# Kernel optimization log

Measured on AMD Instinct MI355X. Metric: run time of the kernel, lower is better.

The kernel has to match this reference:

```python
import jax, jax.numpy as jnp
import numpy as np

DIM = 1024
NUM_HEADS = 16
HEAD_DIM = DIM // NUM_HEADS
SCALE = HEAD_DIM ** -0.5
NEG = -1e9


def setup_inputs() -> dict:
    key = jax.random.key(0)
    ks = jax.random.split(key, 10)
    B, N, M, C = 8, 1024, 1024, DIM
    q = jax.random.normal(ks[0], (B, N, C), jnp.float32)
    k = jax.random.normal(ks[1], (B, M, C), jnp.float32)
    v = jax.random.normal(ks[2], (B, M, C), jnp.float32)
    mask = jax.random.randint(ks[3], (B, N), 0, 2, jnp.int32)
    target_mask = jax.random.randint(ks[4], (B, N, M), 0, 2, jnp.int32)
    Wq = jax.random.normal(ks[5], (C, C), jnp.float32) * 0.02
    Wk = jax.random.normal(ks[6], (C, C), jnp.float32) * 0.02
    Wv = jax.random.normal(ks[7], (C, C), jnp.float32) * 0.02
    Wo = jax.random.normal(ks[8], (C, C), jnp.float32) * 0.02
    bo = jnp.zeros((C,), jnp.float32)
    return {"q": q, "k": k, "v": v, "mask": mask, "target_mask": target_mask,
            "Wq": Wq, "Wk": Wk, "Wv": Wv, "Wo": Wo, "bo": bo}


def reference(q, k, v, mask, target_mask, Wq, Wk, Wv, Wo, bo):
    B, N, C = q.shape
    M = k.shape[1]
    H, D = NUM_HEADS, HEAD_DIM
    qh = (q @ Wq).reshape(B, N, H, D)
    kh = (k @ Wk).reshape(B, M, H, D)
    vh = (v @ Wv).reshape(B, M, H, D)
    attn = jnp.einsum('bnhd,bmhd->bhnm', qh, kh) * SCALE  # (B,H,N,M)
    # self-attn key mask (B,N) -> broadcast over queries (requires N==M as in original)
    attn = jnp.where(mask[:, None, None, :] == 0, NEG, attn)
    # cross-attn mask (B,N,M) -> broadcast over heads
    attn = jnp.where(target_mask[:, None, :, :] == 0, NEG, attn)
    attn = jax.nn.softmax(attn, axis=-1)
    x = jnp.einsum('bhnm,bmhd->bnhd', attn, vh).reshape(B, N, C)
    return x @ Wo + bo
```

## Files before the change

### kernel.cpp

```cpp
#include <hip/hip_runtime.h>
#include <hip/hip_bf16.h>

#define DEV __device__ __forceinline__

typedef __attribute__((ext_vector_type(8))) short bf16x8;
typedef __attribute__((ext_vector_type(4))) float f32x4;
typedef unsigned int u32;
typedef unsigned long long u64;

DEV short f2bf(float f) {
  union { float f; u32 u; } x; x.f = f;
  u32 r = x.u + 0x7fffu + ((x.u >> 16) & 1u);
  return (short)(r >> 16);
}

DEV void gload_lds16(const void* g, void* l) {
  __builtin_amdgcn_global_load_lds(
      (const __attribute__((address_space(1))) u32*)g,
      (__attribute__((address_space(3))) u32*)l, 16, 0, 0);
}

DEV void stage_t128(const char* base, int ktb, char* lds, int w, int lane) {
  int r8 = lane >> 3;
  int csw = ((lane & 7) ^ r8) << 4;
#pragma unroll
  for (int i = 0; i < 4; ++i) {
    int c = w * 4 + i;
    gload_lds16(base + (size_t)(c * 8 + r8) * 2048 + ktb + csw, lds + c * 1024);
  }
}

DEV bf16x8 frag(const short* L, int row, int col) {
  return *(const bf16x8*)&L[row * 64 + (col ^ ((row & 7) << 3))];
}

__global__ __launch_bounds__(256) void aconv(const float* __restrict__ q,
    const float* __restrict__ k, const float* __restrict__ v,
    short* __restrict__ qb, short* __restrict__ kb, short* __restrict__ vb) {
  const float* src; short* dst;
  if (blockIdx.z == 0)      { src = q; dst = qb; }
  else if (blockIdx.z == 1) { src = k; dst = kb; }
  else                      { src = v; dst = vb; }
  size_t i = ((size_t)blockIdx.x * 256 + threadIdx.x) * 8;
  float4 f0 = *(const float4*)(src + i);
  float4 f1 = *(const float4*)(src + i + 4);
  bf16x8 o;
  o[0] = f2bf(f0.x); o[1] = f2bf(f0.y); o[2] = f2bf(f0.z); o[3] = f2bf(f0.w);
  o[4] = f2bf(f1.x); o[5] = f2bf(f1.y); o[6] = f2bf(f1.z); o[7] = f2bf(f1.w);
  *(bf16x8*)(dst + i) = o;
}

__global__ __launch_bounds__(256) void pack_mask(const int* __restrict__ mask,
                                                 const int* __restrict__ tmask,
                                                 u64* __restrict__ pk) {
  int bn = blockIdx.x;
  int b = bn >> 10;
  int t = threadIdx.x, w = t >> 6, lane = t & 63;
  const int* tr = tmask + (size_t)bn * 1024;
  const int* mr = mask + b * 1024;
#pragma unroll
  for (int it = 0; it < 4; ++it) {
    int m = it * 256 + w * 64 + lane;
    bool on = (mr[m] != 0) && (tr[m] != 0);
    u64 bits = __ballot(on);
    if (lane == 0) pk[(size_t)bn * 16 + it * 4 + w] = bits;
  }
}

__global__ __launch_bounds__(256) void wconv4(const float* __restrict__ W0,
    const float* __restrict__ W1, const float* __restrict__ W2,
    const float* __restrict__ W3, short* __restrict__ WtAll) {
  const float* W = blockIdx.z == 0 ? W0 : blockIdx.z == 1 ? W1
                 : blockIdx.z == 2 ? W2 : W3;
  short* Wt = WtAll + (size_t)blockIdx.z * 1024 * 1024;
  __shared__ short tile[64][65];
  int k0 = blockIdx.x * 64, n0 = blockIdx.y * 64;
  int t = threadIdx.x;
  int r = t >> 2, c = (t & 3) * 16;
  const float* src = W + (size_t)(k0 + r) * 1024 + n0 + c;
#pragma unroll
  for (int i = 0; i < 16; i += 4) {
    float4 f = *(const float4*)(src + i);
    tile[r][c + i + 0] = f2bf(f.x);
    tile[r][c + i + 1] = f2bf(f.y);
    tile[r][c + i + 2] = f2bf(f.z);
    tile[r][c + i + 3] = f2bf(f.w);
  }
  __syncthreads();
  bf16x8 v0, v1;
#pragma unroll
  for (int i = 0; i < 8; ++i) v0[i] = tile[c + i][r];
#pragma unroll
  for (int i = 0; i < 8; ++i) v1[i] = tile[c + 8 + i][r];
  short* dst = Wt + (size_t)(n0 + r) * 1024 + k0 + c;
  *(bf16x8*)(dst) = v0;
  *(bf16x8*)(dst + 8) = v1;
}

__global__ __launch_bounds__(256) void vtrans(const short* __restrict__ vh,
                                              short* __restrict__ vht) {
  __shared__ short tile[64][65];
  int m0 = blockIdx.x * 64;
  int bh = blockIdx.y;
  int t = threadIdx.x;
  int r = t >> 2, c = (t & 3) * 16;
  const short* src = vh + ((size_t)bh * 1024 + m0 + r) * 64 + c;
  bf16x8 a0 = *(const bf16x8*)(src);
  bf16x8 a1 = *(const bf16x8*)(src + 8);
#pragma unroll
  for (int i = 0; i < 8; ++i) tile[r][c + i] = a0[i];
#pragma unroll
  for (int i = 0; i < 8; ++i) tile[r][c + 8 + i] = a1[i];
  __syncthreads();
  bf16x8 v0, v1;
#pragma unroll
  for (int i = 0; i < 8; ++i) v0[i] = tile[c + i][r];
#pragma unroll
  for (int i = 0; i < 8; ++i) v1[i] = tile[c + 8 + i][r];
  short* dst = vht + ((size_t)bh * 64 + r) * 1024 + m0 + c;
  *(bf16x8*)dst = v0;
  *(bf16x8*)(dst + 8) = v1;
}

#define QSCALE 0.18033688011112042f

__global__ __launch_bounds__(256, 2) void gemm_qkv(
    const short* __restrict__ qb, const short* __restrict__ kb, const short* __restrict__ vb,
    const short* __restrict__ WtAll,
    short* __restrict__ qh, short* __restrict__ kh, short* __restrict__ vh) {
  int flat = blockIdx.z * 512 + blockIdx.y * 8 + blockIdx.x;
  int nid = (flat & 7) * 192 + (flat >> 3);
  int zz = nid >> 9;
  int rr = nid & 511;
  int bm = (rr >> 3) * 128, bn = (rr & 7) * 128;

  const short* A; short* Ch; float cs;
  if (zz == 0)      { A = qb; Ch = qh; cs = QSCALE; }
  else if (zz == 1) { A = kb; Ch = kh; cs = 1.0f; }
  else              { A = vb; Ch = vh; cs = 1.0f; }
  const short* Wt = WtAll + (size_t)zz * 1024 * 1024;

  __shared__ __align__(16) short As[128 * 64];
  __shared__ __align__(16) short Bs[128 * 64];

  int tid = threadIdx.x;
  int lane = tid & 63, w = tid >> 6;
  int wm = w >> 1, wn = w & 1;
  int lr = lane & 15, lg = lane >> 4;

  const f32x4 fz = {0.f, 0.f, 0.f, 0.f};
  f32x4 acc[4][4];
#pragma unroll
  for (int i = 0; i < 4; ++i)
#pragma unroll
    for (int j = 0; j < 4; ++j) acc[i][j] = fz;

  const char* abase = (const char*)A + (size_t)bm * 2048;
  const char* bbase = (const char*)Wt + (size_t)bn * 2048;

  for (int ktb = 0; ktb < 2048; ktb += 128) {
    stage_t128(abase, ktb, (char*)As, w, lane);
    stage_t128(bbase, ktb, (char*)Bs, w, lane);
    __syncthreads();
#pragma unroll
    for (int ks = 0; ks < 2; ++ks) {
      bf16x8 af[4], bfr[4];
#pragma unroll
      for (int mi = 0; mi < 4; ++mi)
        af[mi] = frag(As, wm * 64 + mi * 16 + lr, ks * 32 + lg * 8);
#pragma unroll
      for (int ni = 0; ni < 4; ++ni)
        bfr[ni] = frag(Bs, wn * 64 + ni * 16 + lr, ks * 32 + lg * 8);
#pragma unroll
      for (int mi = 0; mi < 4; ++mi)
#pragma unroll
        for (int ni = 0; ni < 4; ++ni)
          acc[mi][ni] = __builtin_amdgcn_mfma_f32_16x16x32_bf16(af[mi], bfr[ni], acc[mi][ni], 0, 0, 0);
    }
    __syncthreads();
  }
#pragma unroll
  for (int mi = 0; mi < 4; ++mi)
#pragma unroll
    for (int ni = 0; ni < 4; ++ni) {
      int ccol = bn + wn * 64 + ni * 16 + lr;
      int h = ccol >> 6, d = ccol & 63;
#pragma unroll
      for (int j = 0; j < 4; ++j) {
        int r = bm + wm * 64 + mi * 16 + lg * 4 + j;
        int bb = r >> 10, n = r & 1023;
        Ch[(((size_t)bb * 16 + h) * 1024 + n) * 64 + d] = f2bf(acc[mi][ni][j] * cs);
      }
    }
}

DEV void stage_kv(const char* kbase, const char* vbase, int kv0,
                  short* Ksb, short* Vsb, int w, int lane) {
#pragma unroll
  for (int i = 0; i < 2; ++i) {
    int c = w * 2 + i;
    int row = (lane >> 3);
    int colb = ((lane & 7) ^ row) << 4;
    gload_lds16(kbase + (size_t)(kv0 + c * 8 + row) * 128 + colb, (char*)Ksb + c * 1024);
    gload_lds16(vbase + (size_t)(c * 8 + row) * 2048 + kv0 * 2 + colb, (char*)Vsb + c * 1024);
  }
}

__global__ __launch_bounds__(256, 2) void attn(
    const short* __restrict__ qh, const short* __restrict__ kh, const short* __restrict__ vht,
    const u64* __restrict__ pk, short* __restrict__ x) {
  __shared__ __align__(16) short Ks[2][4096];
  __shared__ __align__(16) short Vs[2][4096];
  __shared__ __align__(16) short Ps[8192];

  int flat = blockIdx.y * 8 + blockIdx.x;
  int nid = (flat & 7) * 128 + (flat >> 3);
  int bh = nid >> 3, qt = nid & 7;
  int b = bh >> 4;
  int tid = threadIdx.x, lane = tid & 63, w = tid >> 6;
  int lr = lane & 15, lg = lane >> 4;

  bf16x8 qa[2][2];
  {
    const short* qb2 = qh + ((size_t)bh * 1024 + qt * 128 + w * 32) * 64;
#pragma unroll
    for (int mi = 0; mi < 2; ++mi)
#pragma unroll
      for (int ks = 0; ks < 2; ++ks)
        qa[mi][ks] = *(const bf16x8*)(qb2 + (mi * 16 + lr) * 64 + ks * 32 + lg * 8);
  }

  const f32x4 fz = {0.f, 0.f, 0.f, 0.f};
  f32x4 o[2][4];
  float psum[2][4];
#pragma unroll
  for (int mi = 0; mi < 2; ++mi)
#pragma unroll
    for (int j = 0; j < 4; ++j) psum[mi][j] = 0.f;
#pragma unroll
  for (int mi = 0; mi < 2; ++mi)
#pragma unroll
    for (int nd = 0; nd < 4; ++nd) o[mi][nd] = fz;

  const char* kbase = (const char*)(kh + (size_t)bh * 65536);
  const char* vbase = (const char*)(vht + (size_t)bh * 65536);
  const u64* pkb = pk + ((size_t)b * 1024 + qt * 128) * 16;

  stage_kv(kbase, vbase, 0, Ks[0], Vs[0], w, lane);
  __syncthreads();
  int cur = 0;

  for (int t = 0; t < 16; ++t) {
    if (t < 15) stage_kv(kbase, vbase, (t + 1) * 64, Ks[cur ^ 1], Vs[cur ^ 1], w, lane);

    u64 pw[2][4];
#pragma unroll
    for (int mi = 0; mi < 2; ++mi)
#pragma unroll
      for (int j = 0; j < 4; ++j)
        pw[mi][j] = pkb[(w * 32 + mi * 16 + lg * 4 + j) * 16 + t];

    f32x4 s[2][4];
#pragma unroll
    for (int mi = 0; mi < 2; ++mi)
#pragma unroll
      for (int ni = 0; ni < 4; ++ni) s[mi][ni] = fz;
#pragma unroll
    for (int ks = 0; ks < 2; ++ks) {
      bf16x8 kb2[4];
#pragma unroll
      for (int ni = 0; ni < 4; ++ni)
        kb2[ni] = *(const bf16x8*)&Ks[cur][(ni * 16 + lr) * 64 + ((ks * 32 + lg * 8) ^ ((lr & 7) << 3))];
#pragma unroll
      for (int mi = 0; mi < 2; ++mi)
#pragma unroll
        for (int ni = 0; ni < 4; ++ni)
          s[mi][ni] = __builtin_amdgcn_mfma_f32_16x16x32_bf16(qa[mi][ks], kb2[ni], s[mi][ni], 0, 0, 0);
    }

#pragma unroll
    for (int mi = 0; mi < 2; ++mi)
#pragma unroll
      for (int j = 0; j < 4; ++j) {
        u32 lo = (u32)pw[mi][j], hi = (u32)(pw[mi][j] >> 32);
        float rs = 0.f;
#pragma unroll
        for (int ni = 0; ni < 4; ++ni) {
          u32 bit = ((ni < 2 ? lo : hi) >> ((ni & 1) * 16 + lr)) & 1u;
          float e = __builtin_amdgcn_exp2f(s[mi][ni][j]);
          float p = bit ? e : 0.f;
          s[mi][ni][j] = p;
          rs += p;
        }
        psum[mi][j] += rs;
      }

#pragma unroll
    for (int mi = 0; mi < 2; ++mi)
#pragma unroll
      for (int j = 0; j < 4; ++j) {
        int r = w * 32 + mi * 16 + lg * 4 + j;
        int sw = (r & 7) << 3;
#pragma unroll
        for (int ni = 0; ni < 4; ++ni)
          Ps[r * 64 + ((ni * 16 + lr) ^ sw)] = f2bf(s[mi][ni][j]);
      }

#pragma unroll
    for (int ks = 0; ks < 2; ++ks) {
      bf16x8 pa[2], vb2[4];
#pragma unroll
      for (int mi = 0; mi < 2; ++mi)
        pa[mi] = *(const bf16x8*)&Ps[(w * 32 + mi * 16 + lr) * 64 + ((ks * 32 + lg * 8) ^ ((lr & 7) << 3))];
#pragma unroll
      for (int nd = 0; nd < 4; ++nd)
        vb2[nd] = *(const bf16x8*)&Vs[cur][(nd * 16 + lr) * 64 + ((ks * 32 + lg * 8) ^ ((lr & 7) << 3))];
#pragma unroll
      for (int mi = 0; mi < 2; ++mi)
#pragma unroll
        for (int nd = 0; nd < 4; ++nd)
          o[mi][nd] = __builtin_amdgcn_mfma_f32_16x16x32_bf16(pa[mi], vb2[nd], o[mi][nd], 0, 0, 0);
    }
    __syncthreads();
    cur ^= 1;
  }

  short* xb = x + ((size_t)b * 1024) * 1024 + (bh & 15) * 64;
#pragma unroll
  for (int mi = 0; mi < 2; ++mi)
#pragma unroll
    for (int j = 0; j < 4; ++j) {
      float rs = psum[mi][j];
#pragma unroll
      for (int dd = 1; dd < 16; dd <<= 1) rs += __shfl_xor(rs, dd, 64);
      float inv = rs > 0.f ? 1.0f / rs : 0.f;
      int qg = qt * 128 + w * 32 + mi * 16 + lg * 4 + j;
#pragma unroll
      for (int nd = 0; nd < 4; ++nd) {
        int d = nd * 16 + lr;
        xb[(size_t)qg * 1024 + d] = f2bf(o[mi][nd][j] * inv);
      }
    }
}

__global__ __launch_bounds__(256, 2) void gemm_out(
    const short* __restrict__ X, const short* __restrict__ Wot,
    const float* __restrict__ bo, float* __restrict__ out) {
  int flat = blockIdx.y * 8 + blockIdx.x;
  int nid = (flat & 7) * 64 + (flat >> 3);
  int bm = (nid >> 3) * 128, bn = (nid & 7) * 128;

  __shared__ __align__(16) short As[128 * 64];
  __shared__ __align__(16) short Bs[128 * 64];
  int tid = threadIdx.x, lane = tid & 63, w = tid >> 6;
  int wm = w >> 1, wn = w & 1, lr = lane & 15, lg = lane >> 4;

  const f32x4 fz = {0.f, 0.f, 0.f, 0.f};
  f32x4 acc[4][4];
#pragma unroll
  for (int i = 0; i < 4; ++i)
#pragma unroll
    for (int j = 0; j < 4; ++j) acc[i][j] = fz;

  const char* abase = (const char*)X + (size_t)bm * 2048;
  const char* bbase = (const char*)Wot + (size_t)bn * 2048;

  for (int ktb = 0; ktb < 2048; ktb += 128) {
    stage_t128(abase, ktb, (char*)As, w, lane);
    stage_t128(bbase, ktb, (char*)Bs, w, lane);
    __syncthreads();
#pragma unroll
    for (int ks = 0; ks < 2; ++ks) {
      bf16x8 af[4], bfr[4];
#pragma unroll
      for (int mi = 0; mi < 4; ++mi)
        af[mi] = frag(As, wm * 64 + mi * 16 + lr, ks * 32 + lg * 8);
#pragma unroll
      for (int ni = 0; ni < 4; ++ni)
        bfr[ni] = frag(Bs, wn * 64 + ni * 16 + lr, ks * 32 + lg * 8);
#pragma unroll
      for (int mi = 0; mi < 4; ++mi)
#pragma unroll
        for (int ni = 0; ni < 4; ++ni)
          acc[mi][ni] = __builtin_amdgcn_mfma_f32_16x16x32_bf16(af[mi], bfr[ni], acc[mi][ni], 0, 0, 0);
    }
    __syncthreads();
  }
#pragma unroll
  for (int mi = 0; mi < 4; ++mi)
#pragma unroll
    for (int ni = 0; ni < 4; ++ni) {
      int ccol = bn + wn * 64 + ni * 16 + lr;
      float bias = bo[ccol];
#pragma unroll
      for (int j = 0; j < 4; ++j) {
        int r = bm + wm * 64 + mi * 16 + lg * 4 + j;
        out[(size_t)r * 1024 + ccol] = acc[mi][ni][j] + bias;
      }
    }
}

extern "C" void kernel_launch(void* const* d_in, const int* in_sizes, int n_in,
                              void* d_out, int out_size, void* d_ws, size_t ws_size,
                              hipStream_t stream) {
  const float* q = (const float*)d_in[0];
  const float* k = (const float*)d_in[1];
  const float* v = (const float*)d_in[2];
  const int* mask = (const int*)d_in[3];
  const int* tmask = (const int*)d_in[4];
  const float* Wq = (const float*)d_in[5];
  const float* Wk = (const float*)d_in[6];
  const float* Wv = (const float*)d_in[7];
  const float* Wo = (const float*)d_in[8];
  const float* bo = (const float*)d_in[9];
  float* out = (float*)d_out;

  char* ws = (char*)d_ws;
  const size_t MB = 1u << 20;
  if (ws_size < 73 * MB) return;
  short* WtAll = (short*)(ws + 0 * MB);
  short* qh  = (short*)(ws + 8 * MB);
  short* kh  = (short*)(ws + 24 * MB);
  short* vh  = (short*)(ws + 40 * MB);
  short* vht = (short*)(ws + 56 * MB);
  u64*   pkb = (u64*)(ws + 72 * MB);
  short* x   = (short*)(ws + 40 * MB);
  short* qbA = (short*)d_out;
  short* kbA = (short*)d_out + 8 * 1024 * 1024;
  short* vbA = (short*)(ws + 56 * MB);

  aconv<<<dim3(4096, 1, 3), 256, 0, stream>>>(q, k, v, qbA, kbA, vbA);
  wconv4<<<dim3(16, 16, 4), 256, 0, stream>>>(Wq, Wk, Wv, Wo, WtAll);
  pack_mask<<<dim3(8192), 256, 0, stream>>>(mask, tmask, pkb);

  gemm_qkv<<<dim3(8, 64, 3), 256, 0, stream>>>(qbA, kbA, vbA, WtAll, qh, kh, vh);
  vtrans<<<dim3(16, 128), 256, 0, stream>>>(vh, vht);
  attn<<<dim3(8, 128), 256, 0, stream>>>(qh, kh, vht, pkb, x);
  gemm_out<<<dim3(8, 64), 256, 0, stream>>>(x, WtAll + 3 * 1024 * 1024, bo, out);
}
```

Measured before the change: 350.7 us.

## Merge prologue kernels, compute V transposed in GEMM, widen attention blocks

Folds the three conversion and mask-packing kernels into one prologue launch. The V projection is now computed as Wv^T·v^T so the GEMM writes the transposed V layout directly, which removes the separate vtrans kernel and its round trip through memory. Attention blocks grow to 512 threads covering 256 queries, so each K/V tile staged in LDS is shared by twice as many query rows. The kernel also adds s_setprio around the MFMA phases and switches the P conversion to a cheaper rounding. In exchange, the transposed V writes are strided, and the simpler rounding slightly changes numerics.

```diff
diff --git a/kernel.cpp b/kernel.cpp
--- a/kernel.cpp
+++ b/kernel.cpp
@@ -34,92 +34,66 @@
   return *(const bf16x8*)&L[row * 64 + (col ^ ((row & 7) << 3))];
 }
 
-__global__ __launch_bounds__(256) void aconv(const float* __restrict__ q,
-    const float* __restrict__ k, const float* __restrict__ v,
-    short* __restrict__ qb, short* __restrict__ kb, short* __restrict__ vb) {
-  const float* src; short* dst;
-  if (blockIdx.z == 0)      { src = q; dst = qb; }
-  else if (blockIdx.z == 1) { src = k; dst = kb; }
-  else                      { src = v; dst = vb; }
-  size_t i = ((size_t)blockIdx.x * 256 + threadIdx.x) * 8;
-  float4 f0 = *(const float4*)(src + i);
-  float4 f1 = *(const float4*)(src + i + 4);
-  bf16x8 o;
-  o[0] = f2bf(f0.x); o[1] = f2bf(f0.y); o[2] = f2bf(f0.z); o[3] = f2bf(f0.w);
-  o[4] = f2bf(f1.x); o[5] = f2bf(f1.y); o[6] = f2bf(f1.z); o[7] = f2bf(f1.w);
-  *(bf16x8*)(dst + i) = o;
-}
-
-__global__ __launch_bounds__(256) void pack_mask(const int* __restrict__ mask,
-                                                 const int* __restrict__ tmask,
-                                                 u64* __restrict__ pk) {
-  int bn = blockIdx.x;
-  int b = bn >> 10;
-  int t = threadIdx.x, w = t >> 6, lane = t & 63;
-  const int* tr = tmask + (size_t)bn * 1024;
-  const int* mr = mask + b * 1024;
-#pragma unroll
-  for (int it = 0; it < 4; ++it) {
-    int m = it * 256 + w * 64 + lane;
-    bool on = (mr[m] != 0) && (tr[m] != 0);
-    u64 bits = __ballot(on);
-    if (lane == 0) pk[(size_t)bn * 16 + it * 4 + w] = bits;
-  }
-}
-
-__global__ __launch_bounds__(256) void wconv4(const float* __restrict__ W0,
-    const float* __restrict__ W1, const float* __restrict__ W2,
-    const float* __restrict__ W3, short* __restrict__ WtAll) {
-  const float* W = blockIdx.z == 0 ? W0 : blockIdx.z == 1 ? W1
-                 : blockIdx.z == 2 ? W2 : W3;
-  short* Wt = WtAll + (size_t)blockIdx.z * 1024 * 1024;
-  __shared__ short tile[64][65];
-  int k0 = blockIdx.x * 64, n0 = blockIdx.y * 64;
-  int t = threadIdx.x;
-  int r = t >> 2, c = (t & 3) * 16;
-  const float* src = W + (size_t)(k0 + r) * 1024 + n0 + c;
-#pragma unroll
-  for (int i = 0; i < 16; i += 4) {
-    float4 f = *(const float4*)(src + i);
-    tile[r][c + i + 0] = f2bf(f.x);
-    tile[r][c + i + 1] = f2bf(f.y);
-    tile[r][c + i + 2] = f2bf(f.z);
-    tile[r][c + i + 3] = f2bf(f.w);
-  }
-  __syncthreads();
-  bf16x8 v0, v1;
-#pragma unroll
-  for (int i = 0; i < 8; ++i) v0[i] = tile[c + i][r];
-#pragma unroll
-  for (int i = 0; i < 8; ++i) v1[i] = tile[c + 8 + i][r];
-  short* dst = Wt + (size_t)(n0 + r) * 1024 + k0 + c;
-  *(bf16x8*)(dst) = v0;
-  *(bf16x8*)(dst + 8) = v1;
-}
-
-__global__ __launch_bounds__(256) void vtrans(const short* __restrict__ vh,
-                                              short* __restrict__ vht) {
-  __shared__ short tile[64][65];
-  int m0 = blockIdx.x * 64;
-  int bh = blockIdx.y;
-  int t = threadIdx.x;
-  int r = t >> 2, c = (t & 3) * 16;
-  const short* src = vh + ((size_t)bh * 1024 + m0 + r) * 64 + c;
-  bf16x8 a0 = *(const bf16x8*)(src);
-  bf16x8 a1 = *(const bf16x8*)(src + 8);
-#pragma unroll
-  for (int i = 0; i < 8; ++i) tile[r][c + i] = a0[i];
-#pragma unroll
-  for (int i = 0; i < 8; ++i) tile[r][c + 8 + i] = a1[i];
-  __syncthreads();
-  bf16x8 v0, v1;
-#pragma unroll
-  for (int i = 0; i < 8; ++i) v0[i] = tile[c + i][r];
-#pragma unroll
-  for (int i = 0; i < 8; ++i) v1[i] = tile[c + 8 + i][r];
-  short* dst = vht + ((size_t)bh * 64 + r) * 1024 + m0 + c;
-  *(bf16x8*)dst = v0;
-  *(bf16x8*)(dst + 8) = v1;
+__global__ __launch_bounds__(256) void prologue(
+    const float* __restrict__ q, const float* __restrict__ k, const float* __restrict__ v,
+    short* __restrict__ qb, short* __restrict__ kb, short* __restrict__ vb,
+    const float* __restrict__ W0, const float* __restrict__ W1,
+    const float* __restrict__ W2, const float* __restrict__ W3,
+    short* __restrict__ WtAll,
+    const int* __restrict__ mask, const int* __restrict__ tmask, u64* __restrict__ pk) {
+  int bx = blockIdx.x;
+  if (bx < 12288) {
+    int z = bx >> 12, bi = bx & 4095;
+    const float* src = z == 0 ? q : z == 1 ? k : v;
+    short* dst = z == 0 ? qb : z == 1 ? kb : vb;
+    size_t i = ((size_t)bi * 256 + threadIdx.x) * 8;
+    float4 f0 = *(const float4*)(src + i);
+    float4 f1 = *(const float4*)(src + i + 4);
+    bf16x8 o;
+    o[0] = f2bf(f0.x); o[1] = f2bf(f0.y); o[2] = f2bf(f0.z); o[3] = f2bf(f0.w);
+    o[4] = f2bf(f1.x); o[5] = f2bf(f1.y); o[6] = f2bf(f1.z); o[7] = f2bf(f1.w);
+    *(bf16x8*)(dst + i) = o;
+  } else if (bx < 13312) {
+    int idx = bx - 12288;
+    int z = idx >> 8, rem = idx & 255;
+    const float* W = z == 0 ? W0 : z == 1 ? W1 : z == 2 ? W2 : W3;
+    short* Wt = WtAll + (size_t)z * 1024 * 1024;
+    __shared__ short tile[64][65];
+    int k0 = (rem >> 4) * 64, n0 = (rem & 15) * 64;
+    int t = threadIdx.x;
+    int r = t >> 2, c = (t & 3) * 16;
+    const float* src = W + (size_t)(k0 + r) * 1024 + n0 + c;
+#pragma unroll
+    for (int i = 0; i < 16; i += 4) {
+      float4 f = *(const float4*)(src + i);
+      tile[r][c + i + 0] = f2bf(f.x);
+      tile[r][c + i + 1] = f2bf(f.y);
+      tile[r][c + i + 2] = f2bf(f.z);
+      tile[r][c + i + 3] = f2bf(f.w);
+    }
+    __syncthreads();
+    bf16x8 v0, v1;
+#pragma unroll
+    for (int i = 0; i < 8; ++i) v0[i] = tile[c + i][r];
+#pragma unroll
+    for (int i = 0; i < 8; ++i) v1[i] = tile[c + 8 + i][r];
+    short* dst = Wt + (size_t)(n0 + r) * 1024 + k0 + c;
+    *(bf16x8*)(dst) = v0;
+    *(bf16x8*)(dst + 8) = v1;
+  } else {
+    int bn = bx - 13312;
+    int b = bn >> 10;
+    int t = threadIdx.x, w = t >> 6, lane = t & 63;
+    const int* tr = tmask + (size_t)bn * 1024;
+    const int* mr = mask + b * 1024;
+#pragma unroll
+    for (int it = 0; it < 4; ++it) {
+      int m = it * 256 + w * 64 + lane;
+      bool on = (mr[m] != 0) && (tr[m] != 0);
+      u64 bits = __ballot(on);
+      if (lane == 0) pk[(size_t)bn * 16 + it * 4 + w] = bits;
+    }
+  }
 }
 
 #define QSCALE 0.18033688011112042f
@@ -127,18 +101,20 @@
 __global__ __launch_bounds__(256, 2) void gemm_qkv(
     const short* __restrict__ qb, const short* __restrict__ kb, const short* __restrict__ vb,
     const short* __restrict__ WtAll,
-    short* __restrict__ qh, short* __restrict__ kh, short* __restrict__ vh) {
-  int flat = blockIdx.z * 512 + blockIdx.y * 8 + blockIdx.x;
+    short* __restrict__ qh, short* __restrict__ kh, short* __restrict__ vht) {
+  int flat = blockIdx.y * 8 + blockIdx.x;
   int nid = (flat & 7) * 192 + (flat >> 3);
   int zz = nid >> 9;
   int rr = nid & 511;
-  int bm = (rr >> 3) * 128, bn = (rr & 7) * 128;
-
-  const short* A; short* Ch; float cs;
-  if (zz == 0)      { A = qb; Ch = qh; cs = QSCALE; }
-  else if (zz == 1) { A = kb; Ch = kh; cs = 1.0f; }
-  else              { A = vb; Ch = vh; cs = 1.0f; }
-  const short* Wt = WtAll + (size_t)zz * 1024 * 1024;
+
+  const short* A; const short* Bw; float cs = 1.0f;
+  int bm, bn;
+  if (zz == 0)      { A = qb; Bw = WtAll;                cs = QSCALE;
+                      bm = (rr >> 3) * 128; bn = (rr & 7) * 128; }
+  else if (zz == 1) { A = kb; Bw = WtAll + 1048576;
+                      bm = (rr >> 3) * 128; bn = (rr & 7) * 128; }
+  else              { A = WtAll + 2 * 1048576; Bw = vb;
+                      bm = (rr >> 6) * 128; bn = (rr & 63) * 128; }
 
   __shared__ __align__(16) short As[128 * 64];
   __shared__ __align__(16) short Bs[128 * 64];
@@ -156,7 +132,7 @@
     for (int j = 0; j < 4; ++j) acc[i][j] = fz;
 
   const char* abase = (const char*)A + (size_t)bm * 2048;
-  const char* bbase = (const char*)Wt + (size_t)bn * 2048;
+  const char* bbase = (const char*)Bw + (size_t)bn * 2048;
 
   for (int ktb = 0; ktb < 2048; ktb += 128) {
     stage_t128(abase, ktb, (char*)As, w, lane);
@@ -179,168 +155,37 @@
     }
     __syncthreads();
   }
-#pragma unroll
-  for (int mi = 0; mi < 4; ++mi)
-#pragma unroll
-    for (int ni = 0; ni < 4; ++ni) {
-      int ccol = bn + wn * 64 + ni * 16 + lr;
-      int h = ccol >> 6, d = ccol & 63;
-#pragma unroll
-      for (int j = 0; j < 4; ++j) {
-        int r = bm + wm * 64 + mi * 16 + lg * 4 + j;
-        int bb = r >> 10, n = r & 1023;
-        Ch[(((size_t)bb * 16 + h) * 1024 + n) * 64 + d] = f2bf(acc[mi][ni][j] * cs);
+
+  if (zz < 2) {
+    short* Ch = (zz == 0) ? qh : kh;
+#pragma unroll
+    for (int mi = 0; mi < 4; ++mi)
+#pragma unroll
+      for (int ni = 0; ni < 4; ++ni) {
+        int ccol = bn + wn * 64 + ni * 16 + lr;
+        int h = ccol >> 6, d = ccol & 63;
+#pragma unroll
+        for (int j = 0; j < 4; ++j) {
+          int r = bm + wm * 64 + mi * 16 + lg * 4 + j;
+          int bb = r >> 10, n = r & 1023;
+          Ch[(((size_t)bb * 16 + h) * 1024 + n) * 64 + d] = f2bf(acc[mi][ni][j] * cs);
+        }
       }
-    }
-}
-
-DEV void stage_kv(const char* kbase, const char* vbase, int kv0,
-                  short* Ksb, short* Vsb, int w, int lane) {
-#pragma unroll
-  for (int i = 0; i < 2; ++i) {
-    int c = w * 2 + i;
-    int row = (lane >> 3);
-    int colb = ((lane & 7) ^ row) << 4;
-    gload_lds16(kbase + (size_t)(kv0 + c * 8 + row) * 128 + colb, (char*)Ksb + c * 1024);
-    gload_lds16(vbase + (size_t)(c * 8 + row) * 2048 + kv0 * 2 + colb, (char*)Vsb + c * 1024);
-  }
-}
-
-__global__ __launch_bounds__(256, 2) void attn(
-    const short* __restrict__ qh, const short* __restrict__ kh, const short* __restrict__ vht,
-    const u64* __restrict__ pk, short* __restrict__ x) {
-  __shared__ __align__(16) short Ks[2][4096];
-  __shared__ __align__(16) short Vs[2][4096];
-  __shared__ __align__(16) short Ps[8192];
-
-  int flat = blockIdx.y * 8 + blockIdx.x;
-  int nid = (flat & 7) * 128 + (flat >> 3);
-  int bh = nid >> 3, qt = nid & 7;
-  int b = bh >> 4;
-  int tid = threadIdx.x, lane = tid & 63, w = tid >> 6;
-  int lr = lane & 15, lg = lane >> 4;
-
-  bf16x8 qa[2][2];
-  {
-    const short* qb2 = qh + ((size_t)bh * 1024 + qt * 128 + w * 32) * 64;
-#pragma unroll
-    for (int mi = 0; mi < 2; ++mi)
-#pragma unroll
-      for (int ks = 0; ks < 2; ++ks)
-        qa[mi][ks] = *(const bf16x8*)(qb2 + (mi * 16 + lr) * 64 + ks * 32 + lg * 8);
-  }
-
-  const f32x4 fz = {0.f, 0.f, 0.f, 0.f};
-  f32x4 o[2][4];
-  float psum[2][4];
-#pragma unroll
-  for (int mi = 0; mi < 2; ++mi)
-#pragma unroll
-    for (int j = 0; j < 4; ++j) psum[mi][j] = 0.f;
-#pragma unroll
-  for (int mi = 0; mi < 2; ++mi)
-#pragma unroll
-    for (int nd = 0; nd < 4; ++nd) o[mi][nd] = fz;
-
-  const char* kbase = (const char*)(kh + (size_t)bh * 65536);
-  const char* vbase = (const char*)(vht + (size_t)bh * 65536);
-  const u64* pkb = pk + ((size_t)b * 1024 + qt * 128) * 16;
-
-  stage_kv(kbase, vbase, 0, Ks[0], Vs[0], w, lane);
-  __syncthreads();
-  int cur = 0;
-
-  for (int t = 0; t < 16; ++t) {
-    if (t < 15) stage_kv(kbase, vbase, (t + 1) * 64, Ks[cur ^ 1], Vs[cur ^ 1], w, lane);
-
-    u64 pw[2][4];
-#pragma unroll
-    for (int mi = 0; mi < 2; ++mi)
-#pragma unroll
-      for (int j = 0; j < 4; ++j)
-        pw[mi][j] = pkb[(w * 32 + mi * 16 + lg * 4 + j) * 16 + t];
-
-    f32x4 s[2][4];
-#pragma unroll
-    for (int mi = 0; mi < 2; ++mi)
-#pragma unroll
-      for (int ni = 0; ni < 4; ++ni) s[mi][ni] = fz;
-#pragma unroll
-    for (int ks = 0; ks < 2; ++ks) {
-      bf16x8 kb2[4];
-#pragma unroll
-      for (int ni = 0; ni < 4; ++ni)
-        kb2[ni] = *(const bf16x8*)&Ks[cur][(ni * 16 + lr) * 64 + ((ks * 32 + lg * 8) ^ ((lr & 7) << 3))];
-#pragma unroll
-      for (int mi = 0; mi < 2; ++mi)
-#pragma unroll
-        for (int ni = 0; ni < 4; ++ni)
-          s[mi][ni] = __builtin_amdgcn_mfma_f32_16x16x32_bf16(qa[mi][ks], kb2[ni], s[mi][ni], 0, 0, 0);
-    }
-
-#pragma unroll
-    for (int mi = 0; mi < 2; ++mi)
-#pragma unroll
-      for (int j = 0; j < 4; ++j) {
-        u32 lo = (u32)pw[mi][j], hi = (u32)(pw[mi][j] >> 32);
-        float rs = 0.f;
-#pragma unroll
-        for (int ni = 0; ni < 4; ++ni) {
-          u32 bit = ((ni < 2 ? lo : hi) >> ((ni & 1) * 16 + lr)) & 1u;
-          float e = __builtin_amdgcn_exp2f(s[mi][ni][j]);
-          float p = bit ? e : 0.f;
-          s[mi][ni][j] = p;
-          rs += p;
+  } else {
+#pragma unroll
+    for (int mi = 0; mi < 4; ++mi)
+#pragma unroll
+      for (int ni = 0; ni < 4; ++ni) {
+        int ccol = bn + wn * 64 + ni * 16 + lr;
+        int bb = ccol >> 10, n = ccol & 1023;
+#pragma unroll
+        for (int j = 0; j < 4; ++j) {
+          int r = bm + wm * 64 + mi * 16 + lg * 4 + j;
+          int h = r >> 6, dd = r & 63;
+          vht[((size_t)bb * 16 + h) * 65536 + dd * 1024 + n] = f2bf(acc[mi][ni][j]);
         }
-        psum[mi][j] += rs;
       }
-
-#pragma unroll
-    for (int mi = 0; mi < 2; ++mi)
-#pragma unroll
-      for (int j = 0; j < 4; ++j) {
-        int r = w * 32 + mi * 16 + lg * 4 + j;
-        int sw = (r & 7) << 3;
-#pragma unroll
-        for (int ni = 0; ni < 4; ++ni)
-          Ps[r * 64 + ((ni * 16 + lr) ^ sw)] = f2bf(s[mi][ni][j]);
-      }
-
-#pragma unroll
-    for (int ks = 0; ks < 2; ++ks) {
-      bf16x8 pa[2], vb2[4];
-#pragma unroll
-      for (int mi = 0; mi < 2; ++mi)
-        pa[mi] = *(const bf16x8*)&Ps[(w * 32 + mi * 16 + lr) * 64 + ((ks * 32 + lg * 8) ^ ((lr & 7) << 3))];
-#pragma unroll
-      for (int nd = 0; nd < 4; ++nd)
-        vb2[nd] = *(const bf16x8*)&Vs[cur][(nd * 16 + lr) * 64 + ((ks * 32 + lg * 8) ^ ((lr & 7) << 3))];
-#pragma unroll
-      for (int mi = 0; mi < 2; ++mi)
-#pragma unroll
-        for (int nd = 0; nd < 4; ++nd)
-          o[mi][nd] = __builtin_amdgcn_mfma_f32_16x16x32_bf16(pa[mi], vb2[nd], o[mi][nd], 0, 0, 0);
-    }
-    __syncthreads();
-    cur ^= 1;
-  }
-
-  short* xb = x + ((size_t)b * 1024) * 1024 + (bh & 15) * 64;
-#pragma unroll
-  for (int mi = 0; mi < 2; ++mi)
-#pragma unroll
-    for (int j = 0; j < 4; ++j) {
-      float rs = psum[mi][j];
-#pragma unroll
-      for (int dd = 1; dd < 16; dd <<= 1) rs += __shfl_xor(rs, dd, 64);
-      float inv = rs > 0.f ? 1.0f / rs : 0.f;
-      int qg = qt * 128 + w * 32 + mi * 16 + lg * 4 + j;
-#pragma unroll
-      for (int nd = 0; nd < 4; ++nd) {
-        int d = nd * 16 + lr;
-        xb[(size_t)qg * 1024 + d] = f2bf(o[mi][nd][j] * inv);
-      }
-    }
+  }
 }
 
 __global__ __launch_bounds__(256, 2) void gemm_out(
@@ -396,6 +241,143 @@
       for (int j = 0; j < 4; ++j) {
         int r = bm + wm * 64 + mi * 16 + lg * 4 + j;
         out[(size_t)r * 1024 + ccol] = acc[mi][ni][j] + bias;
+      }
+    }
+}
+
+DEV void stage_kv8(const char* kbase, const char* vbase, int kv0,
+                   short* Ksb, short* Vsb, int w, int lane) {
+  int row = lane >> 3;
+  int colb = ((lane & 7) ^ row) << 4;
+  gload_lds16(kbase + (size_t)(kv0 + w * 8 + row) * 128 + colb, (char*)Ksb + w * 1024);
+  gload_lds16(vbase + (size_t)(w * 8 + row) * 2048 + kv0 * 2 + colb, (char*)Vsb + w * 1024);
+}
+
+__global__ __launch_bounds__(512, 4) void attn(
+    const short* __restrict__ qh, const short* __restrict__ kh, const short* __restrict__ vht,
+    const u64* __restrict__ pk, short* __restrict__ x) {
+  __shared__ __align__(16) short Ks[2][4096];
+  __shared__ __align__(16) short Vs[2][4096];
+  __shared__ __align__(16) short Ps[256 * 64];
+
+  int flat = blockIdx.y * 8 + blockIdx.x;
+  int nid = (flat & 7) * 64 + (flat >> 3);
+  int bh = nid >> 2, qp = nid & 3;
+  int b = bh >> 4;
+  int tid = threadIdx.x, lane = tid & 63, w = tid >> 6;
+  int lr = lane & 15, lg = lane >> 4;
+
+  bf16x8 qa[2][2];
+  {
+    const short* qb2 = qh + ((size_t)bh * 1024 + qp * 256 + w * 32) * 64;
+#pragma unroll
+    for (int mi = 0; mi < 2; ++mi)
+#pragma unroll
+      for (int ks = 0; ks < 2; ++ks)
+        qa[mi][ks] = *(const bf16x8*)(qb2 + (mi * 16 + lr) * 64 + ks * 32 + lg * 8);
+  }
+
+  const f32x4 fz = {0.f, 0.f, 0.f, 0.f};
+  f32x4 o[2][4];
+  float psum[2][4];
+#pragma unroll
+  for (int mi = 0; mi < 2; ++mi)
+#pragma unroll
+    for (int j = 0; j < 4; ++j) { psum[mi][j] = 0.f; o[mi][j] = fz; }
+
+  const char* kbase = (const char*)(kh + (size_t)bh * 65536);
+  const char* vbase = (const char*)(vht + (size_t)bh * 65536);
+  const u64* pkb = pk + ((size_t)b * 1024 + qp * 256) * 16;
+
+  stage_kv8(kbase, vbase, 0, Ks[0], Vs[0], w, lane);
+  __syncthreads();
+  int cur = 0;
+
+  for (int t = 0; t < 16; ++t) {
+    if (t < 15) stage_kv8(kbase, vbase, (t + 1) * 64, Ks[cur ^ 1], Vs[cur ^ 1], w, lane);
+
+    u64 pw[2][4];
+#pragma unroll
+    for (int mi = 0; mi < 2; ++mi)
+#pragma unroll
+      for (int j = 0; j < 4; ++j)
+        pw[mi][j] = pkb[(w * 32 + mi * 16 + lg * 4 + j) * 16 + t];
+
+    f32x4 s[2][4];
+#pragma unroll
+    for (int mi = 0; mi < 2; ++mi)
+#pragma unroll
+      for (int ni = 0; ni < 4; ++ni) s[mi][ni] = fz;
+    __builtin_amdgcn_s_setprio(1);
+#pragma unroll
+    for (int ks = 0; ks < 2; ++ks) {
+      bf16x8 kb2[4];
+#pragma unroll
+      for (int ni = 0; ni < 4; ++ni)
+        kb2[ni] = *(const bf16x8*)&Ks[cur][(ni * 16 + lr) * 64 + ((ks * 32 + lg * 8) ^ ((lr & 7) << 3))];
+#pragma unroll
+      for (int mi = 0; mi < 2; ++mi)
+#pragma unroll
+        for (int ni = 0; ni < 4; ++ni)
+          s[mi][ni] = __builtin_amdgcn_mfma_f32_16x16x32_bf16(qa[mi][ks], kb2[ni], s[mi][ni], 0, 0, 0);
+    }
+    __builtin_amdgcn_s_setprio(0);
+
+#pragma unroll
+    for (int mi = 0; mi < 2; ++mi)
+#pragma unroll
+      for (int j = 0; j < 4; ++j) {
+        u32 lo = (u32)pw[mi][j], hi = (u32)(pw[mi][j] >> 32);
+        int r = w * 32 + mi * 16 + lg * 4 + j;
+        int sw = (r & 7) << 3;
+        float rs = 0.f;
+#pragma unroll
+        for (int ni = 0; ni < 4; ++ni) {
+          u32 bit = ((ni < 2 ? lo : hi) >> ((ni & 1) * 16 + lr)) & 1u;
+          float e = __builtin_amdgcn_exp2f(s[mi][ni][j]);
+          float p = bit ? e : 0.f;
+          rs += p;
+          union { float f; u32 u; } cv; cv.f = p;
+          Ps[r * 64 + ((ni * 16 + lr) ^ sw)] = (short)((cv.u + 0x8000u) >> 16);
+        }
+        psum[mi][j] += rs;
+      }
+
+    __builtin_amdgcn_s_setprio(1);
+#pragma unroll
+    for (int ks = 0; ks < 2; ++ks) {
+      bf16x8 pa[2], vb2[4];
+#pragma unroll
+      for (int mi = 0; mi < 2; ++mi)
+        pa[mi] = *(const bf16x8*)&Ps[(w * 32 + mi * 16 + lr) * 64 + ((ks * 32 + lg * 8) ^ ((lr & 7) << 3))];
+#pragma unroll
+      for (int nd = 0; nd < 4; ++nd)
+        vb2[nd] = *(const bf16x8*)&Vs[cur][(nd * 16 + lr) * 64 + ((ks * 32 + lg * 8) ^ ((lr & 7) << 3))];
+#pragma unroll
+      for (int mi = 0; mi < 2; ++mi)
+#pragma unroll
+        for (int nd = 0; nd < 4; ++nd)
+          o[mi][nd] = __builtin_amdgcn_mfma_f32_16x16x32_bf16(pa[mi], vb2[nd], o[mi][nd], 0, 0, 0);
+    }
+    __builtin_amdgcn_s_setprio(0);
+    __syncthreads();
+    cur ^= 1;
+  }
+
+  short* xb = x + ((size_t)b * 1024) * 1024 + (bh & 15) * 64;
+#pragma unroll
+  for (int mi = 0; mi < 2; ++mi)
+#pragma unroll
+    for (int j = 0; j < 4; ++j) {
+      float rs = psum[mi][j];
+#pragma unroll
+      for (int dd = 1; dd < 16; dd <<= 1) rs += __shfl_xor(rs, dd, 64);
+      float inv = rs > 0.f ? 1.0f / rs : 0.f;
+      int qg = qp * 256 + w * 32 + mi * 16 + lg * 4 + j;
+#pragma unroll
+      for (int nd = 0; nd < 4; ++nd) {
+        int d = nd * 16 + lr;
+        xb[(size_t)qg * 1024 + d] = f2bf(o[mi][nd][j] * inv);
       }
     }
 }
@@ -421,20 +403,17 @@
   short* WtAll = (short*)(ws + 0 * MB);
   short* qh  = (short*)(ws + 8 * MB);
   short* kh  = (short*)(ws + 24 * MB);
-  short* vh  = (short*)(ws + 40 * MB);
+  short* vb  = (short*)(ws + 40 * MB);
   short* vht = (short*)(ws + 56 * MB);
   u64*   pkb = (u64*)(ws + 72 * MB);
   short* x   = (short*)(ws + 40 * MB);
   short* qbA = (short*)d_out;
   short* kbA = (short*)d_out + 8 * 1024 * 1024;
-  short* vbA = (short*)(ws + 56 * MB);
-
-  aconv<<<dim3(4096, 1, 3), 256, 0, stream>>>(q, k, v, qbA, kbA, vbA);
-  wconv4<<<dim3(16, 16, 4), 256, 0, stream>>>(Wq, Wk, Wv, Wo, WtAll);
-  pack_mask<<<dim3(8192), 256, 0, stream>>>(mask, tmask, pkb);
-
-  gemm_qkv<<<dim3(8, 64, 3), 256, 0, stream>>>(qbA, kbA, vbA, WtAll, qh, kh, vh);
-  vtrans<<<dim3(16, 128), 256, 0, stream>>>(vh, vht);
-  attn<<<dim3(8, 128), 256, 0, stream>>>(qh, kh, vht, pkb, x);
+
+  prologue<<<dim3(21504), 256, 0, stream>>>(q, k, v, qbA, kbA, vb,
+                                            Wq, Wk, Wv, Wo, WtAll,
+                                            mask, tmask, pkb);
+  gemm_qkv<<<dim3(8, 192), 256, 0, stream>>>(qbA, kbA, vb, WtAll, qh, kh, vht);
+  attn<<<dim3(8, 64), 512, 0, stream>>>(qh, kh, vht, pkb, x);
   gemm_out<<<dim3(8, 64), 256, 0, stream>>>(x, WtAll + 3 * 1024 * 1024, bo, out);
 }
```

Measured after the change: 493.0 us. 40.6% more time.
